# Performance work log

Measured on AMD Instinct MI355X. Metric: run time of the kernel, lower is better.

## Reference

```python
import jax, jax.numpy as jnp
import numpy as np

N_POINTS = 500_000
NUM_SUPERNODES = 8192
MAX_DEGREE = 32
HIDDEN = 192
NDIM = 3
INPUT_DIM = 3
MAX_WAVELENGTH = 10000.0


def setup_inputs() -> dict:
    key = jax.random.key(0)
    k = jax.random.split(key, 8)
    rng = np.random.default_rng(0)
    # supernodes: unique node indices; each supernode gets MAX_DEGREE neighbor edges
    supernode_idx = np.sort(rng.choice(N_POINTS, size=NUM_SUPERNODES, replace=False))
    dst_idx = np.repeat(supernode_idx, MAX_DEGREE)              # [E] destination node ids
    src_idx = rng.integers(0, N_POINTS, size=NUM_SUPERNODES * MAX_DEGREE)  # [E] source node ids
    return {
        "input_feat": jax.random.normal(k[0], (N_POINTS, INPUT_DIM), dtype=jnp.float32),
        "input_pos": jax.random.uniform(k[1], (N_POINTS, NDIM), dtype=jnp.float32),
        "src_idx": jnp.asarray(src_idx, dtype=jnp.int64 if jax.config.jax_enable_x64 else jnp.int32),
        "dst_idx": jnp.asarray(dst_idx, dtype=jnp.int64 if jax.config.jax_enable_x64 else jnp.int32),
        "W_in": jax.random.normal(k[2], (INPUT_DIM, HIDDEN), dtype=jnp.float32) * 0.05,
        "b_in": jnp.zeros((HIDDEN,), dtype=jnp.float32),
        "W1": jax.random.normal(k[3], (2 * HIDDEN, HIDDEN), dtype=jnp.float32) * 0.05,
        "b1": jnp.zeros((HIDDEN,), dtype=jnp.float32),
        "W2": jax.random.normal(k[4], (HIDDEN, HIDDEN), dtype=jnp.float32) * 0.05,
        "b2": jnp.zeros((HIDDEN,), dtype=jnp.float32),
    }


def _sincos_embed(pos):
    # ContinuousSincosEmbed: HIDDEN split across NDIM axes, sin/cos halves each
    dim_per_axis = HIDDEN // NDIM  # 64 (even -> no padding)
    omega = 1.0 / MAX_WAVELENGTH ** (
        jnp.arange(0, dim_per_axis, 2, dtype=jnp.float32) / dim_per_axis
    )  # [32]
    ang = pos[:, :, None] * omega  # [N, NDIM, 32]
    emb = jnp.concatenate([jnp.sin(ang), jnp.cos(ang)], axis=-1)  # [N, NDIM, 64]
    return emb.reshape(pos.shape[0], HIDDEN)


def reference(input_feat, input_pos, src_idx, dst_idx, W_in, b_in, W1, b1, W2, b2):
    # node embedding: input projection + continuous sincos positional embed
    x = jnp.dot(input_feat, W_in) + b_in + _sincos_embed(input_pos)  # [N, H]
    # gather + concat edge features: [E, 2H]
    msg = jnp.concatenate([x[src_idx], x[dst_idx]], axis=1)
    # 2-layer message MLP (Linear-GELU-Linear)
    h = jax.nn.gelu(jnp.dot(msg, W1) + b1, approximate=False)
    h = jnp.dot(h, W2) + b2  # [E, H]
    # segment-mean over destination supernodes (fixed degree -> uniform counts)
    E = src_idx.shape[0]
    S = E // MAX_DEGREE
    seg = jnp.repeat(jnp.arange(S), MAX_DEGREE)
    pooled = jax.ops.segment_sum(h, seg, num_segments=S) / MAX_DEGREE  # [S, H]
    return pooled[None]  # [batch_size=1, S, H]
```

## Files before the change

kernel.cpp:

```cpp
#include <hip/hip_runtime.h>

#define DEG 32
#define SAW 232

typedef _Float16 half8 __attribute__((ext_vector_type(8)));
typedef __fp16 fp16x2 __attribute__((ext_vector_type(2)));
typedef float f32x4 __attribute__((ext_vector_type(4)));
typedef int int4v __attribute__((ext_vector_type(4)));

#define EXP2F(x)   __builtin_amdgcn_exp2f(x)
#define SIN_REV(x) __builtin_amdgcn_sinf(x)
#define COS_REV(x) __builtin_amdgcn_cosf(x)
#define RCPF(x)    __builtin_amdgcn_rcpf(x)
#define INV_2PI    0.15915494309189535f
#define NEG_L2_10K_O32 -0.41524101186092046f

__device__ __forceinline__ float gelu_f(float x){
  float x2 = x * x;
  float t  = __builtin_fmaf(0.10294824f, x2, 2.3022079f);
  float e  = EXP2F(x * t);
  float r  = RCPF(1.0f + e);
  return __builtin_fmaf(-x, r, x);
}

__device__ __forceinline__ int pkh(float a, float b){
  fp16x2 p = __builtin_amdgcn_cvt_pkrtz(a, b);
  return __builtin_bit_cast(int, p);
}

__device__ __forceinline__ float wave_reduce(float v){
  #pragma unroll
  for (int s = 1; s < 64; s <<= 1) v += __shfl_xor(v, s, 64);
  return v;
}

__device__ __forceinline__ void tile_gather(_Float16 (*sA)[SAW], float (*sPos)[3],
    float* sOmg, const int* __restrict__ idx, int idx_stride, int base,
    const float* __restrict__ feat, const float* __restrict__ pos, int t){
  if (t < 32) sOmg[t] = EXP2F((float)t * NEG_L2_10K_O32) * INV_2PI;
  if (t < 64){
    int node = idx[(base + t) * idx_stride];
    sPos[t][0] = pos[3*node]; sPos[t][1] = pos[3*node+1]; sPos[t][2] = pos[3*node+2];
  }
  if (t >= 192){
    int e = t - 192;
    int node = idx[(base + e) * idx_stride];
    float f0 = feat[3*node], f1 = feat[3*node+1], f2 = feat[3*node+2];
    int4v v0; v0[0] = pkh(f0, f1); v0[1] = pkh(f2, 0.f); v0[2] = 0; v0[3] = 0;
    int4v z; z[0] = 0; z[1] = 0; z[2] = 0; z[3] = 0;
    *reinterpret_cast<int4v*>(&sA[e][192]) = v0;
    *reinterpret_cast<int4v*>(&sA[e][200]) = z;
    *reinterpret_cast<int4v*>(&sA[e][208]) = z;
    *reinterpret_cast<int4v*>(&sA[e][216]) = z;
  }
}

__device__ __forceinline__ void tile_trig(_Float16 (*sA)[SAW], const float (*sPos)[3],
    const float* sOmg, int t){
  if (t < 192){
    int lane = t & 63, w = t >> 6;
    int r16 = lane & 15, g = lane >> 4;
    float om[8];
    #pragma unroll
    for (int j = 0; j < 8; j++) om[j] = sOmg[8*g + j];
    #pragma unroll
    for (int rr = 0; rr < 4; rr++){
      int row = r16 + rr*16;
      float p = sPos[row][w];
      float a[8];
      #pragma unroll
      for (int j = 0; j < 8; j++) a[j] = p * om[j];
      int4v sv, cv;
      #pragma unroll
      for (int j = 0; j < 4; j++){
        sv[j] = pkh(SIN_REV(a[2*j]), SIN_REV(a[2*j+1]));
        cv[j] = pkh(COS_REV(a[2*j]), COS_REV(a[2*j+1]));
      }
      int ch = w*8 + g;
      *reinterpret_cast<int4v*>(&sA[row][8*ch])     = sv;
      *reinterpret_cast<int4v*>(&sA[row][8*(ch+4)]) = cv;
    }
  }
}

__device__ __forceinline__ void gemm_tile(f32x4 acc[4][3], const _Float16 (*sA)[SAW],
    const _Float16* __restrict__ Bt, int ln15, int grp, int wave){
  #pragma unroll
  for (int k6 = 0; k6 < 7; k6++){
    half8 Af[4];
    #pragma unroll
    for (int m = 0; m < 4; m++)
      Af[m] = *reinterpret_cast<const half8*>(&sA[m*16 + ln15][k6*32 + grp*8]);
    #pragma unroll
    for (int n = 0; n < 3; n++){
      half8 Bf = *reinterpret_cast<const half8*>(Bt + (wave*48 + n*16 + ln15)*224 + k6*32 + grp*8);
      #pragma unroll
      for (int m = 0; m < 4; m++)
        acc[m][n] = __builtin_amdgcn_mfma_f32_16x16x32_f16(Af[m], Bf, acc[m][n], 0, 0, 0);
    }
  }
}

__global__ void k0_prep(const float* __restrict__ W_in, const float* __restrict__ b_in,
    const float* __restrict__ W1, const float* __restrict__ b1,
    const float* __restrict__ W2,
    _Float16* __restrict__ w1tc, _Float16* __restrict__ w1bc,
    _Float16* __restrict__ w2t, float* __restrict__ bias_c){
  int id = blockIdx.x * 256 + threadIdx.x;
  if (id < 86016){
    int half_sel = id / 43008;
    int i = id - half_sel * 43008;
    int n = i / 224, k = i - n * 224;
    const float* Wh = W1 + half_sel * 192 * 192;
    _Float16* dst = half_sel ? w1bc : w1tc;
    if (k < 192)      dst[i] = (_Float16)Wh[k*192 + n];
    else if (k >= 195) dst[i] = (_Float16)0.f;
  } else if (id < 122880){
    int i = id - 86016;
    int n = i / 192, k = i - n * 192;
    w2t[i] = (_Float16)(W2[k*192 + n] * 0.03125f);
  } else if (id < 135168){
    int o = (id - 122880) >> 6, lane = id & 63;
    float s = 0.f;
    #pragma unroll
    for (int u = 0; u < 3; u++){
      int m = lane + 64*u;
      s += b_in[m] * (W1[m*192 + o] + W1[(m+192)*192 + o]);
    }
    s = wave_reduce(s);
    if (lane == 0) bias_c[o] = s + b1[o];
  } else if (id < 208896){
    int o = (id - 135168) >> 6, lane = id & 63;
    int half_sel = o / 576;
    int rem = o - half_sel * 576;
    int r = rem / 192, n = rem - r * 192;
    const float* Wh = W1 + half_sel * 192 * 192;
    float s = 0.f;
    #pragma unroll
    for (int u = 0; u < 3; u++){
      int m = lane + 64*u;
      s += W_in[r*192 + m] * Wh[m*192 + n];
    }
    s = wave_reduce(s);
    if (lane == 0){
      _Float16* dst = half_sel ? w1bc : w1tc;
      dst[n*224 + 192 + r] = (_Float16)s;
    }
  }
}

__global__ __launch_bounds__(256) void k1_dst(const int* __restrict__ dst_idx,
    const float* __restrict__ feat, const float* __restrict__ pos,
    const _Float16* __restrict__ w1bc, const float* __restrict__ bias_c,
    _Float16* __restrict__ a_dst){
  __shared__ _Float16 sA[64][SAW];
  __shared__ float sPos[64][3];
  __shared__ float sOmg[32];
  int blk = blockIdx.x, t = threadIdx.x;
  tile_gather(sA, sPos, sOmg, dst_idx, DEG, blk*64, feat, pos, t);
  __syncthreads();
  tile_trig(sA, sPos, sOmg, t);
  __syncthreads();
  int wave = t >> 6, lane = t & 63, ln15 = lane & 15, grp = lane >> 4;
  f32x4 acc[4][3];
  #pragma unroll
  for (int m = 0; m < 4; m++)
    #pragma unroll
    for (int n = 0; n < 3; n++) acc[m][n] = (f32x4){0.f, 0.f, 0.f, 0.f};
  gemm_tile(acc, sA, w1bc, ln15, grp, wave);
  #pragma unroll
  for (int n = 0; n < 3; n++){
    int col = wave*48 + n*16 + ln15;
    float bias = bias_c[col];
    #pragma unroll
    for (int m = 0; m < 4; m++)
      #pragma unroll
      for (int r = 0; r < 4; r++)
        a_dst[(blk*64 + m*16 + grp*4 + r)*192 + col] = (_Float16)(acc[m][n][r] + bias);
  }
}

__global__ __launch_bounds__(256) void k2_edge(const int* __restrict__ src_idx,
    const float* __restrict__ feat, const float* __restrict__ pos,
    const _Float16* __restrict__ w1tc, const _Float16* __restrict__ a_dst,
    _Float16* __restrict__ S1){
  __shared__ _Float16 sA[64][SAW];
  __shared__ float sPos[64][3];
  __shared__ float sOmg[32];
  int blk = blockIdx.x, t = threadIdx.x;
  int wave = t >> 6, lane = t & 63, ln15 = lane & 15, grp = lane >> 4;

  tile_gather(sA, sPos, sOmg, src_idx, 1, blk*64, feat, pos, t);
  half8 Breg[21];
  {
    const _Float16* bp = w1tc + (wave*48 + ln15)*224 + grp*8;
    #pragma unroll
    for (int n = 0; n < 3; n++)
      #pragma unroll
      for (int k6 = 0; k6 < 7; k6++)
        Breg[n*7 + k6] = *reinterpret_cast<const half8*>(bp + n*16*224 + k6*32);
  }
  __syncthreads();
  tile_trig(sA, sPos, sOmg, t);
  __syncthreads();

  f32x4 acc[4][3];
  #pragma unroll
  for (int m = 0; m < 4; m++)
    #pragma unroll
    for (int n = 0; n < 3; n++) acc[m][n] = (f32x4){0.f, 0.f, 0.f, 0.f};
  #pragma unroll
  for (int k6 = 0; k6 < 7; k6++){
    half8 Af[4];
    #pragma unroll
    for (int m = 0; m < 4; m++)
      Af[m] = *reinterpret_cast<const half8*>(&sA[m*16 + ln15][k6*32 + grp*8]);
    #pragma unroll
    for (int n = 0; n < 3; n++)
      #pragma unroll
      for (int m = 0; m < 4; m++)
        acc[m][n] = __builtin_amdgcn_mfma_f32_16x16x32_f16(Af[m], Breg[n*7 + k6], acc[m][n], 0, 0, 0);
  }

  const _Float16* adp = a_dst + blk*2*192;
  #pragma unroll
  for (int h = 0; h < 2; h++){
    #pragma unroll
    for (int n = 0; n < 3; n++){
      int col = wave*48 + n*16 + ln15;
      float ad = (float)adp[h*192 + col];
      float cs = 0.f;
      #pragma unroll
      for (int mm = 0; mm < 2; mm++){
        f32x4 a = acc[h*2 + mm][n];
        #pragma unroll
        for (int r = 0; r < 4; r++) cs += gelu_f(a[r] + ad);
      }
      cs += __shfl_xor(cs, 16, 64);
      cs += __shfl_xor(cs, 32, 64);
      if (grp == 0)
        S1[(blk*2 + h)*192 + col] = (_Float16)cs;
    }
  }
}

__global__ __launch_bounds__(256) void k3_out(const _Float16* __restrict__ S1,
    const _Float16* __restrict__ w2t, const float* __restrict__ b2,
    float* __restrict__ out){
  int blk = blockIdx.x, t = threadIdx.x;
  int wave = t >> 6, lane = t & 63, ln15 = lane & 15, grp = lane >> 4;
  f32x4 acc[4][3];
  #pragma unroll
  for (int m = 0; m < 4; m++)
    #pragma unroll
    for (int n = 0; n < 3; n++) acc[m][n] = (f32x4){0.f, 0.f, 0.f, 0.f};
  #pragma unroll
  for (int k6 = 0; k6 < 6; k6++){
    half8 Af[4];
    #pragma unroll
    for (int m = 0; m < 4; m++)
      Af[m] = *reinterpret_cast<const half8*>(S1 + (blk*64 + m*16 + ln15)*192 + k6*32 + grp*8);
    #pragma unroll
    for (int n = 0; n < 3; n++){
      half8 Bf = *reinterpret_cast<const half8*>(w2t + (wave*48 + n*16 + ln15)*192 + k6*32 + grp*8);
      #pragma unroll
      for (int m = 0; m < 4; m++)
        acc[m][n] = __builtin_amdgcn_mfma_f32_16x16x32_f16(Af[m], Bf, acc[m][n], 0, 0, 0);
    }
  }
  #pragma unroll
  for (int n = 0; n < 3; n++){
    int col = wave*48 + n*16 + ln15;
    float bias = b2[col];
    #pragma unroll
    for (int m = 0; m < 4; m++)
      #pragma unroll
      for (int r = 0; r < 4; r++)
        out[(blk*64 + m*16 + grp*4 + r)*192 + col] = acc[m][n][r] + bias;
  }
}

extern "C" void kernel_launch(void* const* d_in, const int* in_sizes, int n_in,
                              void* d_out, int out_size, void* d_ws, size_t ws_size,
                              hipStream_t stream) {
  const float* feat   = (const float*)d_in[0];
  const float* pos    = (const float*)d_in[1];
  const int*   src_i  = (const int*)  d_in[2];
  const int*   dst_i  = (const int*)  d_in[3];
  const float* W_in   = (const float*)d_in[4];
  const float* b_in   = (const float*)d_in[5];
  const float* W1     = (const float*)d_in[6];
  const float* b1     = (const float*)d_in[7];
  const float* W2     = (const float*)d_in[8];
  const float* b2     = (const float*)d_in[9];
  float* out = (float*)d_out;

  char* ws = (char*)d_ws;
  _Float16* w1tc   = (_Float16*)(ws);
  _Float16* w1bc   = (_Float16*)(ws + 86016);
  _Float16* w2t    = (_Float16*)(ws + 172032);
  float*    bias_c = (float*)   (ws + 245760);
  _Float16* a_dst  = (_Float16*)(ws + 246528);
  _Float16* S1     = (_Float16*)(ws + 3392256);

  k0_prep<<<816, 256, 0, stream>>>(W_in, b_in, W1, b1, W2, w1tc, w1bc, w2t, bias_c);
  k1_dst <<<128, 256, 0, stream>>>(dst_i, feat, pos, w1bc, bias_c, a_dst);
  k2_edge<<<4096, 256, 0, stream>>>(src_i, feat, pos, w1tc, a_dst, S1);
  k3_out <<<128, 256, 0, stream>>>(S1, w2t, b2, out);
}
```

Measured before the change: 152.3 us.

## Make edge kernel persistent over 8 tiles with double-buffered gather prefetch

The edge kernel now processes 8 consecutive 64-edge tiles per block instead of one. The W1 B-fragments are loaded into registers once per block and reused across all tiles. The next tile's pos/feat gathers are issued into registers before the current tile's trig and MFMA work, then written into a second shared-memory buffer afterwards, so gather latency overlaps compute. The grid drops from 4096 to 512 blocks. Shared memory doubles and fewer blocks can limit occupancy and load balance across CUs.

```diff
diff --git a/kernel.cpp b/kernel.cpp
--- a/kernel.cpp
+++ b/kernel.cpp
@@ -2,6 +2,7 @@
 
 #define DEG 32
 #define SAW 232
+#define TILES 8
 
 typedef _Float16 half8 __attribute__((ext_vector_type(8)));
 typedef __fp16 fp16x2 __attribute__((ext_vector_type(2)));
@@ -32,27 +33,6 @@
   #pragma unroll
   for (int s = 1; s < 64; s <<= 1) v += __shfl_xor(v, s, 64);
   return v;
-}
-
-__device__ __forceinline__ void tile_gather(_Float16 (*sA)[SAW], float (*sPos)[3],
-    float* sOmg, const int* __restrict__ idx, int idx_stride, int base,
-    const float* __restrict__ feat, const float* __restrict__ pos, int t){
-  if (t < 32) sOmg[t] = EXP2F((float)t * NEG_L2_10K_O32) * INV_2PI;
-  if (t < 64){
-    int node = idx[(base + t) * idx_stride];
-    sPos[t][0] = pos[3*node]; sPos[t][1] = pos[3*node+1]; sPos[t][2] = pos[3*node+2];
-  }
-  if (t >= 192){
-    int e = t - 192;
-    int node = idx[(base + e) * idx_stride];
-    float f0 = feat[3*node], f1 = feat[3*node+1], f2 = feat[3*node+2];
-    int4v v0; v0[0] = pkh(f0, f1); v0[1] = pkh(f2, 0.f); v0[2] = 0; v0[3] = 0;
-    int4v z; z[0] = 0; z[1] = 0; z[2] = 0; z[3] = 0;
-    *reinterpret_cast<int4v*>(&sA[e][192]) = v0;
-    *reinterpret_cast<int4v*>(&sA[e][200]) = z;
-    *reinterpret_cast<int4v*>(&sA[e][208]) = z;
-    *reinterpret_cast<int4v*>(&sA[e][216]) = z;
-  }
 }
 
 __device__ __forceinline__ void tile_trig(_Float16 (*sA)[SAW], const float (*sPos)[3],
@@ -157,7 +137,22 @@
   __shared__ float sPos[64][3];
   __shared__ float sOmg[32];
   int blk = blockIdx.x, t = threadIdx.x;
-  tile_gather(sA, sPos, sOmg, dst_idx, DEG, blk*64, feat, pos, t);
+  if (t < 32) sOmg[t] = EXP2F((float)t * NEG_L2_10K_O32) * INV_2PI;
+  if (t < 64){
+    int node = dst_idx[(blk*64 + t) * DEG];
+    sPos[t][0] = pos[3*node]; sPos[t][1] = pos[3*node+1]; sPos[t][2] = pos[3*node+2];
+  }
+  if (t >= 192){
+    int e = t - 192;
+    int node = dst_idx[(blk*64 + e) * DEG];
+    float f0 = feat[3*node], f1 = feat[3*node+1], f2 = feat[3*node+2];
+    int4v v0; v0[0] = pkh(f0, f1); v0[1] = pkh(f2, 0.f); v0[2] = 0; v0[3] = 0;
+    int4v z; z[0] = 0; z[1] = 0; z[2] = 0; z[3] = 0;
+    *reinterpret_cast<int4v*>(&sA[e][192]) = v0;
+    *reinterpret_cast<int4v*>(&sA[e][200]) = z;
+    *reinterpret_cast<int4v*>(&sA[e][208]) = z;
+    *reinterpret_cast<int4v*>(&sA[e][216]) = z;
+  }
   __syncthreads();
   tile_trig(sA, sPos, sOmg, t);
   __syncthreads();
@@ -184,13 +179,15 @@
     const float* __restrict__ feat, const float* __restrict__ pos,
     const _Float16* __restrict__ w1tc, const _Float16* __restrict__ a_dst,
     _Float16* __restrict__ S1){
-  __shared__ _Float16 sA[64][SAW];
-  __shared__ float sPos[64][3];
+  __shared__ _Float16 sA[2][64][SAW];
+  __shared__ float sPos[2][64][3];
   __shared__ float sOmg[32];
   int blk = blockIdx.x, t = threadIdx.x;
   int wave = t >> 6, lane = t & 63, ln15 = lane & 15, grp = lane >> 4;
-
-  tile_gather(sA, sPos, sOmg, src_idx, 1, blk*64, feat, pos, t);
+  int e0 = blk * (TILES*64);
+
+  if (t < 32) sOmg[t] = EXP2F((float)t * NEG_L2_10K_O32) * INV_2PI;
+
   half8 Breg[21];
   {
     const _Float16* bp = w1tc + (wave*48 + ln15)*224 + grp*8;
@@ -200,47 +197,96 @@
       for (int k6 = 0; k6 < 7; k6++)
         Breg[n*7 + k6] = *reinterpret_cast<const half8*>(bp + n*16*224 + k6*32);
   }
+
+  float g0 = 0.f, g1 = 0.f, g2 = 0.f;
+  if (t < 64){
+    int node = src_idx[e0 + t];
+    g0 = pos[3*node]; g1 = pos[3*node+1]; g2 = pos[3*node+2];
+    sPos[0][t][0] = g0; sPos[0][t][1] = g1; sPos[0][t][2] = g2;
+  } else if (t >= 192){
+    int e = t - 192;
+    int node = src_idx[e0 + e];
+    g0 = feat[3*node]; g1 = feat[3*node+1]; g2 = feat[3*node+2];
+    int4v v0; v0[0] = pkh(g0, g1); v0[1] = pkh(g2, 0.f); v0[2] = 0; v0[3] = 0;
+    int4v z; z[0] = 0; z[1] = 0; z[2] = 0; z[3] = 0;
+    *reinterpret_cast<int4v*>(&sA[0][e][192]) = v0;
+    *reinterpret_cast<int4v*>(&sA[0][e][200]) = z;
+    *reinterpret_cast<int4v*>(&sA[0][e][208]) = z;
+    *reinterpret_cast<int4v*>(&sA[0][e][216]) = z;
+  }
   __syncthreads();
-  tile_trig(sA, sPos, sOmg, t);
-  __syncthreads();
-
-  f32x4 acc[4][3];
-  #pragma unroll
-  for (int m = 0; m < 4; m++)
-    #pragma unroll
-    for (int n = 0; n < 3; n++) acc[m][n] = (f32x4){0.f, 0.f, 0.f, 0.f};
-  #pragma unroll
-  for (int k6 = 0; k6 < 7; k6++){
-    half8 Af[4];
-    #pragma unroll
-    for (int m = 0; m < 4; m++)
-      Af[m] = *reinterpret_cast<const half8*>(&sA[m*16 + ln15][k6*32 + grp*8]);
-    #pragma unroll
-    for (int n = 0; n < 3; n++)
+
+  for (int tl = 0; tl < TILES; ++tl){
+    int cur = tl & 1;
+    if (tl + 1 < TILES){
+      if (t < 64){
+        int node = src_idx[e0 + (tl+1)*64 + t];
+        g0 = pos[3*node]; g1 = pos[3*node+1]; g2 = pos[3*node+2];
+      } else if (t >= 192){
+        int node = src_idx[e0 + (tl+1)*64 + (t-192)];
+        g0 = feat[3*node]; g1 = feat[3*node+1]; g2 = feat[3*node+2];
+      }
+    }
+    float ad[2][3];
+    {
+      const _Float16* adp = a_dst + (blk*TILES + tl)*2*192 + wave*48 + ln15;
+      #pragma unroll
+      for (int h = 0; h < 2; h++)
+        #pragma unroll
+        for (int n = 0; n < 3; n++)
+          ad[h][n] = (float)adp[h*192 + n*16];
+    }
+    tile_trig(sA[cur], sPos[cur], sOmg, t);
+    __syncthreads();
+    f32x4 acc[4][3];
+    #pragma unroll
+    for (int m = 0; m < 4; m++)
+      #pragma unroll
+      for (int n = 0; n < 3; n++) acc[m][n] = (f32x4){0.f, 0.f, 0.f, 0.f};
+    #pragma unroll
+    for (int k6 = 0; k6 < 7; k6++){
+      half8 Af[4];
       #pragma unroll
       for (int m = 0; m < 4; m++)
-        acc[m][n] = __builtin_amdgcn_mfma_f32_16x16x32_f16(Af[m], Breg[n*7 + k6], acc[m][n], 0, 0, 0);
-  }
-
-  const _Float16* adp = a_dst + blk*2*192;
-  #pragma unroll
-  for (int h = 0; h < 2; h++){
-    #pragma unroll
-    for (int n = 0; n < 3; n++){
-      int col = wave*48 + n*16 + ln15;
-      float ad = (float)adp[h*192 + col];
-      float cs = 0.f;
-      #pragma unroll
-      for (int mm = 0; mm < 2; mm++){
-        f32x4 a = acc[h*2 + mm][n];
+        Af[m] = *reinterpret_cast<const half8*>(&sA[cur][m*16 + ln15][k6*32 + grp*8]);
+      #pragma unroll
+      for (int n = 0; n < 3; n++)
         #pragma unroll
-        for (int r = 0; r < 4; r++) cs += gelu_f(a[r] + ad);
+        for (int m = 0; m < 4; m++)
+          acc[m][n] = __builtin_amdgcn_mfma_f32_16x16x32_f16(Af[m], Breg[n*7 + k6], acc[m][n], 0, 0, 0);
+    }
+    #pragma unroll
+    for (int h = 0; h < 2; h++){
+      #pragma unroll
+      for (int n = 0; n < 3; n++){
+        float cs = 0.f;
+        #pragma unroll
+        for (int mm = 0; mm < 2; mm++){
+          f32x4 a = acc[h*2 + mm][n];
+          #pragma unroll
+          for (int r = 0; r < 4; r++) cs += gelu_f(a[r] + ad[h][n]);
+        }
+        cs += __shfl_xor(cs, 16, 64);
+        cs += __shfl_xor(cs, 32, 64);
+        if (grp == 0)
+          S1[((blk*TILES + tl)*2 + h)*192 + wave*48 + n*16 + ln15] = (_Float16)cs;
       }
-      cs += __shfl_xor(cs, 16, 64);
-      cs += __shfl_xor(cs, 32, 64);
-      if (grp == 0)
-        S1[(blk*2 + h)*192 + col] = (_Float16)cs;
-    }
+    }
+    if (tl + 1 < TILES){
+      int nxt = cur ^ 1;
+      if (t < 64){
+        sPos[nxt][t][0] = g0; sPos[nxt][t][1] = g1; sPos[nxt][t][2] = g2;
+      } else if (t >= 192){
+        int e = t - 192;
+        int4v v0; v0[0] = pkh(g0, g1); v0[1] = pkh(g2, 0.f); v0[2] = 0; v0[3] = 0;
+        int4v z; z[0] = 0; z[1] = 0; z[2] = 0; z[3] = 0;
+        *reinterpret_cast<int4v*>(&sA[nxt][e][192]) = v0;
+        *reinterpret_cast<int4v*>(&sA[nxt][e][200]) = z;
+        *reinterpret_cast<int4v*>(&sA[nxt][e][208]) = z;
+        *reinterpret_cast<int4v*>(&sA[nxt][e][216]) = z;
+      }
+    }
+    __syncthreads();
   }
 }
 
@@ -305,6 +351,6 @@
 
   k0_prep<<<816, 256, 0, stream>>>(W_in, b_in, W1, b1, W2, w1tc, w1bc, w2t, bias_c);
   k1_dst <<<128, 256, 0, stream>>>(dst_i, feat, pos, w1bc, bias_c, a_dst);
-  k2_edge<<<4096, 256, 0, stream>>>(src_i, feat, pos, w1tc, a_dst, S1);
+  k2_edge<<<512, 256, 0, stream>>>(src_i, feat, pos, w1tc, a_dst, S1);
   k3_out <<<128, 256, 0, stream>>>(S1, w2t, b2, out);
 }
```

Measured after the change: 138.3 us. -9.2%, faster.

## Fuse destination-node projection into edge kernel with multi-tile software pipelining

Applied to the files above, without the earlier changes.

Removes the separate k1_dst kernel and its a_dst buffer. Each edge block now computes the 8 destination supernode projections itself into shared memory, then loops over 4 edge tiles. While one tile is in the GEMM and GELU stages, the gathers for the next tile are prefetched into registers and double-buffered positions. Blocks drop from 4096 to 1024, and B fragments are now read from global or L2 per tile instead of held in registers. This saves a launch and the global round trip of a_dst, at the cost of more syncs per block and fewer blocks.

```diff
diff --git a/kernel.cpp b/kernel.cpp
--- a/kernel.cpp
+++ b/kernel.cpp
@@ -2,6 +2,7 @@
 
 #define DEG 32
 #define SAW 232
+#define NT  4
 
 typedef _Float16 half8 __attribute__((ext_vector_type(8)));
 typedef __fp16 fp16x2 __attribute__((ext_vector_type(2)));
@@ -34,37 +35,19 @@
   return v;
 }
 
-__device__ __forceinline__ void tile_gather(_Float16 (*sA)[SAW], float (*sPos)[3],
-    float* sOmg, const int* __restrict__ idx, int idx_stride, int base,
-    const float* __restrict__ feat, const float* __restrict__ pos, int t){
-  if (t < 32) sOmg[t] = EXP2F((float)t * NEG_L2_10K_O32) * INV_2PI;
-  if (t < 64){
-    int node = idx[(base + t) * idx_stride];
-    sPos[t][0] = pos[3*node]; sPos[t][1] = pos[3*node+1]; sPos[t][2] = pos[3*node+2];
-  }
-  if (t >= 192){
-    int e = t - 192;
-    int node = idx[(base + e) * idx_stride];
-    float f0 = feat[3*node], f1 = feat[3*node+1], f2 = feat[3*node+2];
-    int4v v0; v0[0] = pkh(f0, f1); v0[1] = pkh(f2, 0.f); v0[2] = 0; v0[3] = 0;
-    int4v z; z[0] = 0; z[1] = 0; z[2] = 0; z[3] = 0;
-    *reinterpret_cast<int4v*>(&sA[e][192]) = v0;
-    *reinterpret_cast<int4v*>(&sA[e][200]) = z;
-    *reinterpret_cast<int4v*>(&sA[e][208]) = z;
-    *reinterpret_cast<int4v*>(&sA[e][216]) = z;
-  }
-}
-
+template<int ROWS>
 __device__ __forceinline__ void tile_trig(_Float16 (*sA)[SAW], const float (*sPos)[3],
     const float* sOmg, int t){
   if (t < 192){
     int lane = t & 63, w = t >> 6;
     int r16 = lane & 15, g = lane >> 4;
+    if (ROWS < 16 && r16 >= ROWS) return;
     float om[8];
     #pragma unroll
     for (int j = 0; j < 8; j++) om[j] = sOmg[8*g + j];
-    #pragma unroll
-    for (int rr = 0; rr < 4; rr++){
+    constexpr int NRR = (ROWS >= 16) ? ROWS/16 : 1;
+    #pragma unroll
+    for (int rr = 0; rr < NRR; rr++){
       int row = r16 + rr*16;
       float p = sPos[row][w];
       float a[8];
@@ -79,24 +62,6 @@
       int ch = w*8 + g;
       *reinterpret_cast<int4v*>(&sA[row][8*ch])     = sv;
       *reinterpret_cast<int4v*>(&sA[row][8*(ch+4)]) = cv;
-    }
-  }
-}
-
-__device__ __forceinline__ void gemm_tile(f32x4 acc[4][3], const _Float16 (*sA)[SAW],
-    const _Float16* __restrict__ Bt, int ln15, int grp, int wave){
-  #pragma unroll
-  for (int k6 = 0; k6 < 7; k6++){
-    half8 Af[4];
-    #pragma unroll
-    for (int m = 0; m < 4; m++)
-      Af[m] = *reinterpret_cast<const half8*>(&sA[m*16 + ln15][k6*32 + grp*8]);
-    #pragma unroll
-    for (int n = 0; n < 3; n++){
-      half8 Bf = *reinterpret_cast<const half8*>(Bt + (wave*48 + n*16 + ln15)*224 + k6*32 + grp*8);
-      #pragma unroll
-      for (int m = 0; m < 4; m++)
-        acc[m][n] = __builtin_amdgcn_mfma_f32_16x16x32_f16(Af[m], Bf, acc[m][n], 0, 0, 0);
     }
   }
 }
@@ -149,97 +114,151 @@
   }
 }
 
-__global__ __launch_bounds__(256) void k1_dst(const int* __restrict__ dst_idx,
+__global__ __launch_bounds__(256, 4) void k2_fused(const int* __restrict__ src_idx,
+    const int* __restrict__ dst_idx,
     const float* __restrict__ feat, const float* __restrict__ pos,
-    const _Float16* __restrict__ w1bc, const float* __restrict__ bias_c,
-    _Float16* __restrict__ a_dst){
+    const _Float16* __restrict__ w1tc, const _Float16* __restrict__ w1bc,
+    const float* __restrict__ bias_c, _Float16* __restrict__ S1){
   __shared__ _Float16 sA[64][SAW];
-  __shared__ float sPos[64][3];
-  __shared__ float sOmg[32];
-  int blk = blockIdx.x, t = threadIdx.x;
-  tile_gather(sA, sPos, sOmg, dst_idx, DEG, blk*64, feat, pos, t);
-  __syncthreads();
-  tile_trig(sA, sPos, sOmg, t);
-  __syncthreads();
-  int wave = t >> 6, lane = t & 63, ln15 = lane & 15, grp = lane >> 4;
-  f32x4 acc[4][3];
-  #pragma unroll
-  for (int m = 0; m < 4; m++)
-    #pragma unroll
-    for (int n = 0; n < 3; n++) acc[m][n] = (f32x4){0.f, 0.f, 0.f, 0.f};
-  gemm_tile(acc, sA, w1bc, ln15, grp, wave);
-  #pragma unroll
-  for (int n = 0; n < 3; n++){
-    int col = wave*48 + n*16 + ln15;
-    float bias = bias_c[col];
-    #pragma unroll
-    for (int m = 0; m < 4; m++)
-      #pragma unroll
-      for (int r = 0; r < 4; r++)
-        a_dst[(blk*64 + m*16 + grp*4 + r)*192 + col] = (_Float16)(acc[m][n][r] + bias);
-  }
-}
-
-__global__ __launch_bounds__(256) void k2_edge(const int* __restrict__ src_idx,
-    const float* __restrict__ feat, const float* __restrict__ pos,
-    const _Float16* __restrict__ w1tc, const _Float16* __restrict__ a_dst,
-    _Float16* __restrict__ S1){
-  __shared__ _Float16 sA[64][SAW];
-  __shared__ float sPos[64][3];
+  __shared__ _Float16 sAd[2*NT][192];
+  __shared__ float sPos[2][64][3];
   __shared__ float sOmg[32];
   int blk = blockIdx.x, t = threadIdx.x;
   int wave = t >> 6, lane = t & 63, ln15 = lane & 15, grp = lane >> 4;
-
-  tile_gather(sA, sPos, sOmg, src_idx, 1, blk*64, feat, pos, t);
-  half8 Breg[21];
+  int e0 = blk * (NT*64);
+  int s0 = blk * (NT*2);
+
+  if (t < 32) sOmg[t] = EXP2F((float)t * NEG_L2_10K_O32) * INV_2PI;
+  if (t < 64){
+    int4v z; z[0] = 0; z[1] = 0; z[2] = 0; z[3] = 0;
+    *reinterpret_cast<int4v*>(&sA[t][200]) = z;
+    *reinterpret_cast<int4v*>(&sA[t][208]) = z;
+    *reinterpret_cast<int4v*>(&sA[t][216]) = z;
+  }
+  int idxA[NT];
+  if (t < 64){
+    #pragma unroll
+    for (int tl = 0; tl < NT; tl++) idxA[tl] = src_idx[e0 + tl*64 + t];
+  } else if (t >= 192){
+    #pragma unroll
+    for (int tl = 0; tl < NT; tl++) idxA[tl] = src_idx[e0 + tl*64 + (t-192)];
+  }
+  if (t < 8){
+    int nd = dst_idx[(s0 + t) * DEG];
+    sPos[1][t][0] = pos[3*nd]; sPos[1][t][1] = pos[3*nd+1]; sPos[1][t][2] = pos[3*nd+2];
+  } else if (t >= 192 && t < 200){
+    int e = t - 192;
+    int nd = dst_idx[(s0 + e) * DEG];
+    float f0 = feat[3*nd], f1 = feat[3*nd+1], f2 = feat[3*nd+2];
+    int4v v0; v0[0] = pkh(f0, f1); v0[1] = pkh(f2, 0.f); v0[2] = 0; v0[3] = 0;
+    *reinterpret_cast<int4v*>(&sA[e][192]) = v0;
+  }
+  __syncthreads();
+  tile_trig<8>(sA, sPos[1], sOmg, t);
+  float p0 = 0.f, p1 = 0.f, p2 = 0.f;
+  if (t < 64){
+    int nd = idxA[0];
+    p0 = pos[3*nd]; p1 = pos[3*nd+1]; p2 = pos[3*nd+2];
+  } else if (t >= 192){
+    int nd = idxA[0];
+    p0 = feat[3*nd]; p1 = feat[3*nd+1]; p2 = feat[3*nd+2];
+  }
+  __syncthreads();
   {
-    const _Float16* bp = w1tc + (wave*48 + ln15)*224 + grp*8;
-    #pragma unroll
-    for (int n = 0; n < 3; n++)
-      #pragma unroll
-      for (int k6 = 0; k6 < 7; k6++)
-        Breg[n*7 + k6] = *reinterpret_cast<const half8*>(bp + n*16*224 + k6*32);
-  }
-  __syncthreads();
-  tile_trig(sA, sPos, sOmg, t);
-  __syncthreads();
-
-  f32x4 acc[4][3];
-  #pragma unroll
-  for (int m = 0; m < 4; m++)
-    #pragma unroll
-    for (int n = 0; n < 3; n++) acc[m][n] = (f32x4){0.f, 0.f, 0.f, 0.f};
-  #pragma unroll
-  for (int k6 = 0; k6 < 7; k6++){
-    half8 Af[4];
-    #pragma unroll
-    for (int m = 0; m < 4; m++)
-      Af[m] = *reinterpret_cast<const half8*>(&sA[m*16 + ln15][k6*32 + grp*8]);
-    #pragma unroll
-    for (int n = 0; n < 3; n++)
-      #pragma unroll
-      for (int m = 0; m < 4; m++)
-        acc[m][n] = __builtin_amdgcn_mfma_f32_16x16x32_f16(Af[m], Breg[n*7 + k6], acc[m][n], 0, 0, 0);
-  }
-
-  const _Float16* adp = a_dst + blk*2*192;
-  #pragma unroll
-  for (int h = 0; h < 2; h++){
+    f32x4 a1[3];
+    #pragma unroll
+    for (int n = 0; n < 3; n++) a1[n] = (f32x4){0.f, 0.f, 0.f, 0.f};
+    #pragma unroll
+    for (int k6 = 0; k6 < 7; k6++){
+      half8 Af = *reinterpret_cast<const half8*>(&sA[ln15][k6*32 + grp*8]);
+      #pragma unroll
+      for (int n = 0; n < 3; n++){
+        half8 Bf = *reinterpret_cast<const half8*>(w1bc + (wave*48 + n*16 + ln15)*224 + k6*32 + grp*8);
+        a1[n] = __builtin_amdgcn_mfma_f32_16x16x32_f16(Af, Bf, a1[n], 0, 0, 0);
+      }
+    }
     #pragma unroll
     for (int n = 0; n < 3; n++){
       int col = wave*48 + n*16 + ln15;
-      float ad = (float)adp[h*192 + col];
-      float cs = 0.f;
-      #pragma unroll
-      for (int mm = 0; mm < 2; mm++){
-        f32x4 a = acc[h*2 + mm][n];
+      float bc = bias_c[col];
+      #pragma unroll
+      for (int r = 0; r < 4; r++){
+        int row = grp*4 + r;
+        if (row < 8) sAd[row][col] = (_Float16)(a1[n][r] + bc);
+      }
+    }
+  }
+  __syncthreads();
+  if (t < 64){
+    sPos[0][t][0] = p0; sPos[0][t][1] = p1; sPos[0][t][2] = p2;
+  } else if (t >= 192){
+    int4v v0; v0[0] = pkh(p0, p1); v0[1] = pkh(p2, 0.f); v0[2] = 0; v0[3] = 0;
+    *reinterpret_cast<int4v*>(&sA[t-192][192]) = v0;
+  }
+  __syncthreads();
+
+  for (int tl = 0; tl < NT; ++tl){
+    if (tl + 1 < NT){
+      if (t < 64){
+        int nd = idxA[tl+1];
+        p0 = pos[3*nd]; p1 = pos[3*nd+1]; p2 = pos[3*nd+2];
+      } else if (t >= 192){
+        int nd = idxA[tl+1];
+        p0 = feat[3*nd]; p1 = feat[3*nd+1]; p2 = feat[3*nd+2];
+      }
+    }
+    float ad[2][3];
+    #pragma unroll
+    for (int h = 0; h < 2; h++)
+      #pragma unroll
+      for (int n = 0; n < 3; n++)
+        ad[h][n] = (float)sAd[tl*2 + h][wave*48 + n*16 + ln15];
+    tile_trig<64>(sA, sPos[tl & 1], sOmg, t);
+    __syncthreads();
+    f32x4 acc[4][3];
+    #pragma unroll
+    for (int m = 0; m < 4; m++)
+      #pragma unroll
+      for (int n = 0; n < 3; n++) acc[m][n] = (f32x4){0.f, 0.f, 0.f, 0.f};
+    #pragma unroll
+    for (int k6 = 0; k6 < 7; k6++){
+      half8 Af[4];
+      #pragma unroll
+      for (int m = 0; m < 4; m++)
+        Af[m] = *reinterpret_cast<const half8*>(&sA[m*16 + ln15][k6*32 + grp*8]);
+      #pragma unroll
+      for (int n = 0; n < 3; n++){
+        half8 Bf = *reinterpret_cast<const half8*>(w1tc + (wave*48 + n*16 + ln15)*224 + k6*32 + grp*8);
         #pragma unroll
-        for (int r = 0; r < 4; r++) cs += gelu_f(a[r] + ad);
-      }
-      cs += __shfl_xor(cs, 16, 64);
-      cs += __shfl_xor(cs, 32, 64);
-      if (grp == 0)
-        S1[(blk*2 + h)*192 + col] = (_Float16)cs;
+        for (int m = 0; m < 4; m++)
+          acc[m][n] = __builtin_amdgcn_mfma_f32_16x16x32_f16(Af[m], Bf, acc[m][n], 0, 0, 0);
+      }
+    }
+    #pragma unroll
+    for (int h = 0; h < 2; h++){
+      #pragma unroll
+      for (int n = 0; n < 3; n++){
+        float cs = 0.f;
+        #pragma unroll
+        for (int mm = 0; mm < 2; mm++){
+          f32x4 a = acc[h*2 + mm][n];
+          #pragma unroll
+          for (int r = 0; r < 4; r++) cs += gelu_f(a[r] + ad[h][n]);
+        }
+        cs += __shfl_xor(cs, 16, 64);
+        cs += __shfl_xor(cs, 32, 64);
+        if (grp == 0)
+          S1[(s0 + tl*2 + h)*192 + wave*48 + n*16 + ln15] = (_Float16)cs;
+      }
+    }
+    if (tl + 1 < NT && t < 64){
+      int nxt = (tl+1) & 1;
+      sPos[nxt][t][0] = p0; sPos[nxt][t][1] = p1; sPos[nxt][t][2] = p2;
+    }
+    __syncthreads();
+    if (tl + 1 < NT && t >= 192){
+      int4v v0; v0[0] = pkh(p0, p1); v0[1] = pkh(p2, 0.f); v0[2] = 0; v0[3] = 0;
+      *reinterpret_cast<int4v*>(&sA[t-192][192]) = v0;
     }
   }
 }
@@ -300,11 +319,9 @@
   _Float16* w1bc   = (_Float16*)(ws + 86016);
   _Float16* w2t    = (_Float16*)(ws + 172032);
   float*    bias_c = (float*)   (ws + 245760);
-  _Float16* a_dst  = (_Float16*)(ws + 246528);
-  _Float16* S1     = (_Float16*)(ws + 3392256);
-
-  k0_prep<<<816, 256, 0, stream>>>(W_in, b_in, W1, b1, W2, w1tc, w1bc, w2t, bias_c);
-  k1_dst <<<128, 256, 0, stream>>>(dst_i, feat, pos, w1bc, bias_c, a_dst);
-  k2_edge<<<4096, 256, 0, stream>>>(src_i, feat, pos, w1tc, a_dst, S1);
-  k3_out <<<128, 256, 0, stream>>>(S1, w2t, b2, out);
-}
+  _Float16* S1     = (_Float16*)(ws + 246528);
+
+  k0_prep <<<816, 256, 0, stream>>>(W_in, b_in, W1, b1, W2, w1tc, w1bc, w2t, bias_c);
+  k2_fused<<<1024, 256, 0, stream>>>(src_i, dst_i, feat, pos, w1tc, w1bc, bias_c, S1);
+  k3_out  <<<128, 256, 0, stream>>>(S1, w2t, b2, out);
+}
```

Result: slower. 165.5 us (+8.7%).

## Pack node feat/pos to fp16 table and pipeline persistent multi-tile edge kernel

Applied to the files above, without the earlier changes.

Adds a pass in the prep kernel that packs every node's feat and pos into one 16-byte fp16 record, so each edge gather becomes a single vector load instead of six scalar loads. The edge kernel becomes a 512-thread block that loops over four 128-edge tiles. Two waves prefetch the next tile's packed records while six waves compute the sin/cos embedding, and the accumulators start from the a_dst values so the add before GELU disappears. Weight prep is rewritten for coalesced reads. The cost is an extra full pass over all 500k points, which the kernel now has to do, and pos is rounded to fp16 before the trig, which reduces accuracy.

```diff
diff --git a/kernel.cpp b/kernel.cpp
--- a/kernel.cpp
+++ b/kernel.cpp
@@ -2,6 +2,7 @@
 
 #define DEG 32
 #define SAW 232
+#define NT  4
 
 typedef _Float16 half8 __attribute__((ext_vector_type(8)));
 typedef __fp16 fp16x2 __attribute__((ext_vector_type(2)));
@@ -34,93 +35,34 @@
   return v;
 }
 
-__device__ __forceinline__ void tile_gather(_Float16 (*sA)[SAW], float (*sPos)[3],
-    float* sOmg, const int* __restrict__ idx, int idx_stride, int base,
-    const float* __restrict__ feat, const float* __restrict__ pos, int t){
-  if (t < 32) sOmg[t] = EXP2F((float)t * NEG_L2_10K_O32) * INV_2PI;
-  if (t < 64){
-    int node = idx[(base + t) * idx_stride];
-    sPos[t][0] = pos[3*node]; sPos[t][1] = pos[3*node+1]; sPos[t][2] = pos[3*node+2];
-  }
-  if (t >= 192){
-    int e = t - 192;
-    int node = idx[(base + e) * idx_stride];
-    float f0 = feat[3*node], f1 = feat[3*node+1], f2 = feat[3*node+2];
-    int4v v0; v0[0] = pkh(f0, f1); v0[1] = pkh(f2, 0.f); v0[2] = 0; v0[3] = 0;
-    int4v z; z[0] = 0; z[1] = 0; z[2] = 0; z[3] = 0;
-    *reinterpret_cast<int4v*>(&sA[e][192]) = v0;
-    *reinterpret_cast<int4v*>(&sA[e][200]) = z;
-    *reinterpret_cast<int4v*>(&sA[e][208]) = z;
-    *reinterpret_cast<int4v*>(&sA[e][216]) = z;
-  }
-}
-
-__device__ __forceinline__ void tile_trig(_Float16 (*sA)[SAW], const float (*sPos)[3],
-    const float* sOmg, int t){
-  if (t < 192){
-    int lane = t & 63, w = t >> 6;
-    int r16 = lane & 15, g = lane >> 4;
-    float om[8];
-    #pragma unroll
-    for (int j = 0; j < 8; j++) om[j] = sOmg[8*g + j];
-    #pragma unroll
-    for (int rr = 0; rr < 4; rr++){
-      int row = r16 + rr*16;
-      float p = sPos[row][w];
-      float a[8];
-      #pragma unroll
-      for (int j = 0; j < 8; j++) a[j] = p * om[j];
-      int4v sv, cv;
-      #pragma unroll
-      for (int j = 0; j < 4; j++){
-        sv[j] = pkh(SIN_REV(a[2*j]), SIN_REV(a[2*j+1]));
-        cv[j] = pkh(COS_REV(a[2*j]), COS_REV(a[2*j+1]));
-      }
-      int ch = w*8 + g;
-      *reinterpret_cast<int4v*>(&sA[row][8*ch])     = sv;
-      *reinterpret_cast<int4v*>(&sA[row][8*(ch+4)]) = cv;
-    }
-  }
-}
-
-__device__ __forceinline__ void gemm_tile(f32x4 acc[4][3], const _Float16 (*sA)[SAW],
-    const _Float16* __restrict__ Bt, int ln15, int grp, int wave){
-  #pragma unroll
-  for (int k6 = 0; k6 < 7; k6++){
-    half8 Af[4];
-    #pragma unroll
-    for (int m = 0; m < 4; m++)
-      Af[m] = *reinterpret_cast<const half8*>(&sA[m*16 + ln15][k6*32 + grp*8]);
-    #pragma unroll
-    for (int n = 0; n < 3; n++){
-      half8 Bf = *reinterpret_cast<const half8*>(Bt + (wave*48 + n*16 + ln15)*224 + k6*32 + grp*8);
-      #pragma unroll
-      for (int m = 0; m < 4; m++)
-        acc[m][n] = __builtin_amdgcn_mfma_f32_16x16x32_f16(Af[m], Bf, acc[m][n], 0, 0, 0);
-    }
-  }
-}
-
 __global__ void k0_prep(const float* __restrict__ W_in, const float* __restrict__ b_in,
     const float* __restrict__ W1, const float* __restrict__ b1,
-    const float* __restrict__ W2,
+    const float* __restrict__ W2, const float* __restrict__ feat,
+    const float* __restrict__ pos, int npts,
     _Float16* __restrict__ w1tc, _Float16* __restrict__ w1bc,
-    _Float16* __restrict__ w2t, float* __restrict__ bias_c){
+    _Float16* __restrict__ w2t, float* __restrict__ bias_c,
+    _Float16* __restrict__ pf){
   int id = blockIdx.x * 256 + threadIdx.x;
-  if (id < 86016){
-    int half_sel = id / 43008;
-    int i = id - half_sel * 43008;
-    int n = i / 224, k = i - n * 224;
-    const float* Wh = W1 + half_sel * 192 * 192;
-    _Float16* dst = half_sel ? w1bc : w1tc;
-    if (k < 192)      dst[i] = (_Float16)Wh[k*192 + n];
-    else if (k >= 195) dst[i] = (_Float16)0.f;
-  } else if (id < 122880){
-    int i = id - 86016;
-    int n = i / 192, k = i - n * 192;
-    w2t[i] = (_Float16)(W2[k*192 + n] * 0.03125f);
-  } else if (id < 135168){
-    int o = (id - 122880) >> 6, lane = id & 63;
+  if (id < 73728){
+    int half_sel = id / 36864;
+    int i = id - half_sel * 36864;
+    int k = i / 192, n = i - k * 192;
+    const float* Wh = W1 + half_sel * 36864;
+    (half_sel ? w1bc : w1tc)[n*224 + k] = (_Float16)Wh[i];
+  } else if (id < 84864){
+    int i = id - 73728;
+    int half_sel = i / 5568;
+    int j = i - half_sel * 5568;
+    int n = j / 29, k = 195 + (j - n * 29);
+    (half_sel ? w1bc : w1tc)[n*224 + k] = (_Float16)0.f;
+  } else if (id < 121728){
+    int i = id - 84864;
+    int k = i / 192, n = i - k * 192;
+    w2t[n*192 + k] = (_Float16)(W2[i] * 0.03125f);
+  } else if (id < 134016){
+    int o = (id - 121728 - 12288 + 12288) >> 6;
+    o = (id - 121728) >> 6;
+    int lane = id & 63;
     float s = 0.f;
     #pragma unroll
     for (int u = 0; u < 3; u++){
@@ -129,12 +71,12 @@
     }
     s = wave_reduce(s);
     if (lane == 0) bias_c[o] = s + b1[o];
-  } else if (id < 208896){
-    int o = (id - 135168) >> 6, lane = id & 63;
+  } else if (id < 207744){
+    int o = (id - 134016) >> 6, lane = id & 63;
     int half_sel = o / 576;
     int rem = o - half_sel * 576;
     int r = rem / 192, n = rem - r * 192;
-    const float* Wh = W1 + half_sel * 192 * 192;
+    const float* Wh = W1 + half_sel * 36864;
     float s = 0.f;
     #pragma unroll
     for (int u = 0; u < 3; u++){
@@ -142,9 +84,15 @@
       s += W_in[r*192 + m] * Wh[m*192 + n];
     }
     s = wave_reduce(s);
-    if (lane == 0){
-      _Float16* dst = half_sel ? w1bc : w1tc;
-      dst[n*224 + 192 + r] = (_Float16)s;
+    if (lane == 0) (half_sel ? w1bc : w1tc)[n*224 + 192 + r] = (_Float16)s;
+  } else {
+    int n = id - 207744;
+    if (n < npts){
+      float f0 = feat[3*n], f1 = feat[3*n+1], f2 = feat[3*n+2];
+      float p0 = pos[3*n],  p1 = pos[3*n+1],  p2 = pos[3*n+2];
+      int4v v; v[0] = pkh(f0, f1); v[1] = pkh(f2, 0.f);
+               v[2] = pkh(p0, p1); v[3] = pkh(p2, 0.f);
+      *reinterpret_cast<int4v*>(pf + n*8) = v;
     }
   }
 }
@@ -157,9 +105,45 @@
   __shared__ float sPos[64][3];
   __shared__ float sOmg[32];
   int blk = blockIdx.x, t = threadIdx.x;
-  tile_gather(sA, sPos, sOmg, dst_idx, DEG, blk*64, feat, pos, t);
+  if (t < 32) sOmg[t] = EXP2F((float)t * NEG_L2_10K_O32) * INV_2PI;
+  if (t < 64){
+    int node = dst_idx[(blk*64 + t) * DEG];
+    sPos[t][0] = pos[3*node]; sPos[t][1] = pos[3*node+1]; sPos[t][2] = pos[3*node+2];
+  }
+  if (t >= 192){
+    int e = t - 192;
+    int node = dst_idx[(blk*64 + e) * DEG];
+    float f0 = feat[3*node], f1 = feat[3*node+1], f2 = feat[3*node+2];
+    int4v v0; v0[0] = pkh(f0, f1); v0[1] = pkh(f2, 0.f); v0[2] = 0; v0[3] = 0;
+    int4v z; z[0] = 0; z[1] = 0; z[2] = 0; z[3] = 0;
+    *reinterpret_cast<int4v*>(&sA[e][192]) = v0;
+    *reinterpret_cast<int4v*>(&sA[e][200]) = z;
+    *reinterpret_cast<int4v*>(&sA[e][208]) = z;
+    *reinterpret_cast<int4v*>(&sA[e][216]) = z;
+  }
   __syncthreads();
-  tile_trig(sA, sPos, sOmg, t);
+  if (t < 192){
+    int lane = t & 63, w = t >> 6;
+    int r16 = lane & 15, g = lane >> 4;
+    float om[8];
+    #pragma unroll
+    for (int j = 0; j < 8; j++) om[j] = sOmg[8*g + j];
+    #pragma unroll
+    for (int rr = 0; rr < 4; rr++){
+      int row = r16 + rr*16;
+      float p = sPos[row][w];
+      int4v sv, cv;
+      #pragma unroll
+      for (int j = 0; j < 4; j++){
+        float a0 = p * om[2*j], a1 = p * om[2*j+1];
+        sv[j] = pkh(SIN_REV(a0), SIN_REV(a1));
+        cv[j] = pkh(COS_REV(a0), COS_REV(a1));
+      }
+      int ch = w*8 + g;
+      *reinterpret_cast<int4v*>(&sA[row][8*ch])     = sv;
+      *reinterpret_cast<int4v*>(&sA[row][8*(ch+4)]) = cv;
+    }
+  }
   __syncthreads();
   int wave = t >> 6, lane = t & 63, ln15 = lane & 15, grp = lane >> 4;
   f32x4 acc[4][3];
@@ -167,7 +151,20 @@
   for (int m = 0; m < 4; m++)
     #pragma unroll
     for (int n = 0; n < 3; n++) acc[m][n] = (f32x4){0.f, 0.f, 0.f, 0.f};
-  gemm_tile(acc, sA, w1bc, ln15, grp, wave);
+  #pragma unroll
+  for (int k6 = 0; k6 < 7; k6++){
+    half8 Af[4];
+    #pragma unroll
+    for (int m = 0; m < 4; m++)
+      Af[m] = *reinterpret_cast<const half8*>(&sA[m*16 + ln15][k6*32 + grp*8]);
+    #pragma unroll
+    for (int n = 0; n < 3; n++){
+      half8 Bf = *reinterpret_cast<const half8*>(w1bc + (wave*48 + n*16 + ln15)*224 + k6*32 + grp*8);
+      #pragma unroll
+      for (int m = 0; m < 4; m++)
+        acc[m][n] = __builtin_amdgcn_mfma_f32_16x16x32_f16(Af[m], Bf, acc[m][n], 0, 0, 0);
+    }
+  }
   #pragma unroll
   for (int n = 0; n < 3; n++){
     int col = wave*48 + n*16 + ln15;
@@ -180,67 +177,120 @@
   }
 }
 
-__global__ __launch_bounds__(256) void k2_edge(const int* __restrict__ src_idx,
-    const float* __restrict__ feat, const float* __restrict__ pos,
-    const _Float16* __restrict__ w1tc, const _Float16* __restrict__ a_dst,
-    _Float16* __restrict__ S1){
-  __shared__ _Float16 sA[64][SAW];
-  __shared__ float sPos[64][3];
-  __shared__ float sOmg[32];
+__global__ __launch_bounds__(512) void k2_edge(const int* __restrict__ src_idx,
+    const _Float16* __restrict__ pf, const _Float16* __restrict__ w1tc,
+    const _Float16* __restrict__ a_dst, _Float16* __restrict__ S1){
+  __shared__ _Float16 sA[128][SAW];
+  __shared__ float sPos[128][3];
   int blk = blockIdx.x, t = threadIdx.x;
-  int wave = t >> 6, lane = t & 63, ln15 = lane & 15, grp = lane >> 4;
-
-  tile_gather(sA, sPos, sOmg, src_idx, 1, blk*64, feat, pos, t);
-  half8 Breg[21];
-  {
-    const _Float16* bp = w1tc + (wave*48 + ln15)*224 + grp*8;
-    #pragma unroll
-    for (int n = 0; n < 3; n++)
-      #pragma unroll
-      for (int k6 = 0; k6 < 7; k6++)
-        Breg[n*7 + k6] = *reinterpret_cast<const half8*>(bp + n*16*224 + k6*32);
+  int wv = t >> 6, lane = t & 63, ln15 = lane & 15, grp = lane >> 4;
+  int e0 = blk * (NT*128), sn_base = blk * (NT*4);
+  int mg = wv >> 2, cg = wv & 3;
+
+  float om8[8];
+  #pragma unroll
+  for (int j = 0; j < 8; j++)
+    om8[j] = EXP2F((float)(grp*8 + j) * NEG_L2_10K_O32) * INV_2PI;
+
+  int idxA[NT];
+  half8 vcur, vnxt;
+  if (wv >= 6){
+    int grow = t - 384;
+    #pragma unroll
+    for (int tl = 0; tl < NT; tl++) idxA[tl] = src_idx[e0 + tl*128 + grow];
+    vcur = *reinterpret_cast<const half8*>(pf + idxA[0]*8);
+    int4v z; z[0] = 0; z[1] = 0; z[2] = 0; z[3] = 0;
+    *reinterpret_cast<int4v*>(&sA[grow][200]) = z;
+    *reinterpret_cast<int4v*>(&sA[grow][208]) = z;
+    *reinterpret_cast<int4v*>(&sA[grow][216]) = z;
+    int4v vi = __builtin_bit_cast(int4v, vcur);
+    int4v fv; fv[0] = vi[0]; fv[1] = vi[1]; fv[2] = 0; fv[3] = 0;
+    *reinterpret_cast<int4v*>(&sA[grow][192]) = fv;
+    sPos[grow][0] = (float)vcur[4]; sPos[grow][1] = (float)vcur[5]; sPos[grow][2] = (float)vcur[6];
   }
   __syncthreads();
-  tile_trig(sA, sPos, sOmg, t);
-  __syncthreads();
-
-  f32x4 acc[4][3];
-  #pragma unroll
-  for (int m = 0; m < 4; m++)
-    #pragma unroll
-    for (int n = 0; n < 3; n++) acc[m][n] = (f32x4){0.f, 0.f, 0.f, 0.f};
-  #pragma unroll
-  for (int k6 = 0; k6 < 7; k6++){
-    half8 Af[4];
-    #pragma unroll
-    for (int m = 0; m < 4; m++)
-      Af[m] = *reinterpret_cast<const half8*>(&sA[m*16 + ln15][k6*32 + grp*8]);
-    #pragma unroll
-    for (int n = 0; n < 3; n++)
+
+  for (int tl = 0; tl < NT; ++tl){
+    float ad[2][3];
+    #pragma unroll
+    for (int h = 0; h < 2; h++){
+      int sn = sn_base + tl*4 + mg*2 + h;
+      #pragma unroll
+      for (int n = 0; n < 3; n++)
+        ad[h][n] = (float)a_dst[sn*192 + cg*48 + n*16 + ln15];
+    }
+    if (wv < 6){
+      int axis = wv >> 1, sub = wv & 1;
+      #pragma unroll
+      for (int rr = 0; rr < 4; rr++){
+        int row = ln15 + rr*16 + sub*64;
+        float p = sPos[row][axis];
+        int4v sv, cv;
+        #pragma unroll
+        for (int j = 0; j < 4; j++){
+          float a0 = p * om8[2*j], a1 = p * om8[2*j+1];
+          sv[j] = pkh(SIN_REV(a0), SIN_REV(a1));
+          cv[j] = pkh(COS_REV(a0), COS_REV(a1));
+        }
+        *reinterpret_cast<int4v*>(&sA[row][64*axis + 8*grp])      = sv;
+        *reinterpret_cast<int4v*>(&sA[row][64*axis + 32 + 8*grp]) = cv;
+      }
+    } else {
+      int grow = t - 384;
+      if (tl > 0){
+        int4v vi = __builtin_bit_cast(int4v, vcur);
+        int4v fv; fv[0] = vi[0]; fv[1] = vi[1]; fv[2] = 0; fv[3] = 0;
+        *reinterpret_cast<int4v*>(&sA[grow][192]) = fv;
+      }
+      if (tl + 1 < NT) vnxt = *reinterpret_cast<const half8*>(pf + idxA[tl+1]*8);
+    }
+    __syncthreads();
+    f32x4 acc[4][3];
+    #pragma unroll
+    for (int m = 0; m < 4; m++)
+      #pragma unroll
+      for (int n = 0; n < 3; n++){
+        float av = ad[m>>1][n];
+        acc[m][n] = (f32x4){av, av, av, av};
+      }
+    #pragma unroll
+    for (int k6 = 0; k6 < 7; k6++){
+      half8 Af[4];
       #pragma unroll
       for (int m = 0; m < 4; m++)
-        acc[m][n] = __builtin_amdgcn_mfma_f32_16x16x32_f16(Af[m], Breg[n*7 + k6], acc[m][n], 0, 0, 0);
-  }
-
-  const _Float16* adp = a_dst + blk*2*192;
-  #pragma unroll
-  for (int h = 0; h < 2; h++){
-    #pragma unroll
-    for (int n = 0; n < 3; n++){
-      int col = wave*48 + n*16 + ln15;
-      float ad = (float)adp[h*192 + col];
-      float cs = 0.f;
-      #pragma unroll
-      for (int mm = 0; mm < 2; mm++){
-        f32x4 a = acc[h*2 + mm][n];
+        Af[m] = *reinterpret_cast<const half8*>(&sA[mg*64 + m*16 + ln15][k6*32 + grp*8]);
+      #pragma unroll
+      for (int n = 0; n < 3; n++){
+        half8 Bf = *reinterpret_cast<const half8*>(w1tc + (cg*48 + n*16 + ln15)*224 + k6*32 + grp*8);
         #pragma unroll
-        for (int r = 0; r < 4; r++) cs += gelu_f(a[r] + ad);
-      }
-      cs += __shfl_xor(cs, 16, 64);
-      cs += __shfl_xor(cs, 32, 64);
-      if (grp == 0)
-        S1[(blk*2 + h)*192 + col] = (_Float16)cs;
-    }
+        for (int m = 0; m < 4; m++)
+          acc[m][n] = __builtin_amdgcn_mfma_f32_16x16x32_f16(Af[m], Bf, acc[m][n], 0, 0, 0);
+      }
+    }
+    #pragma unroll
+    for (int h = 0; h < 2; h++){
+      int sn = sn_base + tl*4 + mg*2 + h;
+      #pragma unroll
+      for (int n = 0; n < 3; n++){
+        float cs = 0.f;
+        #pragma unroll
+        for (int mm = 0; mm < 2; mm++){
+          f32x4 a = acc[h*2 + mm][n];
+          #pragma unroll
+          for (int r = 0; r < 4; r++) cs += gelu_f(a[r]);
+        }
+        cs += __shfl_xor(cs, 16, 64);
+        cs += __shfl_xor(cs, 32, 64);
+        if (grp == 0)
+          S1[sn*192 + cg*48 + n*16 + ln15] = (_Float16)cs;
+      }
+    }
+    if (wv >= 6 && tl + 1 < NT){
+      int grow = t - 384;
+      sPos[grow][0] = (float)vnxt[4]; sPos[grow][1] = (float)vnxt[5]; sPos[grow][2] = (float)vnxt[6];
+      vcur = vnxt;
+    }
+    __syncthreads();
   }
 }
 
@@ -294,6 +344,7 @@
   const float* W2     = (const float*)d_in[8];
   const float* b2     = (const float*)d_in[9];
   float* out = (float*)d_out;
+  int npts = in_sizes[0] / 3;
 
   char* ws = (char*)d_ws;
   _Float16* w1tc   = (_Float16*)(ws);
@@ -302,9 +353,12 @@
   float*    bias_c = (float*)   (ws + 245760);
   _Float16* a_dst  = (_Float16*)(ws + 246528);
   _Float16* S1     = (_Float16*)(ws + 3392256);
-
-  k0_prep<<<816, 256, 0, stream>>>(W_in, b_in, W1, b1, W2, w1tc, w1bc, w2t, bias_c);
+  _Float16* pf     = (_Float16*)(ws + 6537984);
+
+  int k0_grid = (207744 + npts + 255) / 256;
+  k0_prep<<<k0_grid, 256, 0, stream>>>(W_in, b_in, W1, b1, W2, feat, pos, npts,
+                                       w1tc, w1bc, w2t, bias_c, pf);
   k1_dst <<<128, 256, 0, stream>>>(dst_i, feat, pos, w1bc, bias_c, a_dst);
-  k2_edge<<<4096, 256, 0, stream>>>(src_i, feat, pos, w1tc, a_dst, S1);
+  k2_edge<<<512, 512, 0, stream>>>(src_i, pf, w1tc, a_dst, S1);
   k3_out <<<128, 256, 0, stream>>>(S1, w2t, b2, out);
 }
```

New measurement: 143.4 us. 5.8% less time.
